# Kernel optimization log

Hardware: AMD Instinct MI355X
Metric: run time of the kernel (lower is better)

The kernel has to match this reference:

```python
import jax, jax.numpy as jnp
import numpy as np
from jax import lax

B, T, V, E, H, W = 4, 1024, 32000, 512, 1024, 8
EPS = 1e-5


def setup_inputs() -> dict:
    key = jax.random.key(0)
    ks = jax.random.split(key, 20)
    s = 0.05
    p = {
        'x': jax.random.randint(ks[0], (B, T), 0, V),
        'emb': jax.random.normal(ks[1], (V, E)) * s,
        # candidate_mlp: Linear(2H+E -> 2H), ReLU, Linear(2H -> H)
        'W1c': jax.random.normal(ks[2], (2 * H + E, 2 * H)) * s,
        'b1c': jnp.zeros((2 * H,)),
        'W2c': jax.random.normal(ks[3], (2 * H, H)) * s,
        'b2c': jnp.zeros((H,)),
        # gate_net: Linear(2H+E -> H), Tanh, Linear(H -> 1), Sigmoid
        'Wg1': jax.random.normal(ks[4], (2 * H + E, H)) * s,
        'bg1': jnp.zeros((H,)),
        'Wg2': jax.random.normal(ks[5], (H, 1)) * s,
        'bg2': jnp.zeros((1,)),
        # res_proj: Linear(E -> H)
        'Wr': jax.random.normal(ks[6], (E, H)) * s,
        'br': jnp.zeros((H,)),
        # attention projections (H -> H)
        'Wk': jax.random.normal(ks[7], (H, H)) * s,
        'bk': jnp.zeros((H,)),
        'Wq': jax.random.normal(ks[8], (H, H)) * s,
        'bq': jnp.zeros((H,)),
        'Wv': jax.random.normal(ks[9], (H, H)) * s,
        'bv': jnp.zeros((H,)),
        # output head (H -> V)
        'Wf': jax.random.normal(ks[10], (H, V)) * s,
        'bf': jnp.zeros((V,)),
    }
    return p


def _layer_norm(h):
    mu = h.mean(-1, keepdims=True)
    var = ((h - mu) ** 2).mean(-1, keepdims=True)
    return (h - mu) * lax.rsqrt(var + EPS)


def _forward(x, emb, W1c, b1c, W2c, b2c, Wg1, bg1, Wg2, bg2, Wr, br,
             Wk, bk, Wq, bq, Wv, bv, Wf, bf):
    e = emb[x]  # [B, T, E]
    h0 = jnp.zeros((B, H), dtype=e.dtype)

    def step(carry, et):
        h2, h1 = carry
        ctx = jnp.concatenate([h1, h2, et], axis=-1)  # [B, 2H+E]
        cand = jnp.maximum(ctx @ W1c + b1c, 0.0) @ W2c + b2c  # [B, H]
        gate = jax.nn.sigmoid(jnp.tanh(ctx @ Wg1 + bg1) @ Wg2 + bg2)  # [B, 1]
        h = h1 + gate * cand + 0.1 * (et @ Wr + br)
        hn = _layer_norm(h)
        return (h1, hn), hn

    _, states = lax.scan(step, (h0, h0), jnp.swapaxes(e, 0, 1))  # [T, B, H]
    states = jnp.swapaxes(states, 0, 1)  # [B, T, H]

    # windowed causal attention: each t attends to [max(0, t-W), t]
    q = states @ Wq + bq  # [B, T, H]
    k = states @ Wk + bk
    v = states @ Wv + bv
    t_idx = jnp.arange(T)[:, None]
    j = jnp.arange(W + 1)[None, :]
    idx = t_idx - W + j            # [T, W+1]
    valid = idx >= 0
    idxc = jnp.clip(idx, 0, T - 1)
    kw = k[:, idxc, :]             # [B, T, W+1, H]
    vw = v[:, idxc, :]
    scores = jnp.einsum('bth,btwh->btw', q, kw) / jnp.sqrt(jnp.asarray(H, q.dtype))
    scores = jnp.where(valid[None], scores, -jnp.inf)
    w = jax.nn.softmax(scores, axis=-1)
    attn = jnp.einsum('btw,btwh->bth', w, vw)  # [B, T, H]
    return attn @ Wf + bf  # [B, T, V]


def reference(x, emb, W1c, b1c, W2c, b2c, Wg1, bg1, Wg2, bg2, Wr, br,
              Wk, bk, Wq, bq, Wv, bv, Wf, bf):
    return _forward(x, emb, W1c, b1c, W2c, b2c, Wg1, bg1, Wg2, bg2, Wr, br,
                    Wk, bk, Wq, bq, Wv, bv, Wf, bf)
```

## Files before the change

kernel.cpp:

```cpp
#include <hip/hip_runtime.h>

typedef unsigned short ushort_t;

constexpr int TT = 1024;

__device__ __forceinline__ float blo(unsigned u) { return __uint_as_float(u << 16); }
__device__ __forceinline__ float bhi(unsigned u) { return __uint_as_float(u & 0xffff0000u); }
__device__ __forceinline__ ushort_t f2bf(float f) {
  unsigned u = __float_as_uint(f);
  unsigned r = (u + 0x7fffu + ((u >> 16) & 1u)) >> 16;
  return (ushort_t)r;
}
__device__ __forceinline__ float tanh_fast(float x) {
  float ax = fabsf(x);
  float e = exp2f(ax * 2.885390081777927f);
  float r = 1.f - 2.f / (e + 1.f);
  return copysignf(r, x);
}

__device__ __forceinline__ void st_agent(float* p, float v) {
  __hip_atomic_store(p, v, __ATOMIC_RELAXED, __HIP_MEMORY_SCOPE_AGENT);
}

__device__ __forceinline__ void ldg_hb4(const float* p0, const float* p1,
                                        const float* p2, const float* p3,
                                        float4& r0, float4& r1, float4& r2, float4& r3)
{
  asm volatile(
    "global_load_dwordx4 %0, %4, off sc0 sc1\n\t"
    "global_load_dwordx4 %1, %5, off sc0 sc1\n\t"
    "global_load_dwordx4 %2, %6, off sc0 sc1\n\t"
    "global_load_dwordx4 %3, %7, off sc0 sc1\n\t"
    "s_waitcnt vmcnt(0)"
    : "=&v"(r0), "=&v"(r1), "=&v"(r2), "=&v"(r3)
    : "v"(p0), "v"(p1), "v"(p2), "v"(p3)
    : "memory");
}

__device__ __forceinline__ void ldg_phase2(
    const float* gbase, const float* cbase,
    float4& g0, float4& g1, float4& g2, float4& g3,
    float4& a0, float4& a1, float4& a2, float4& a3,
    float4& a4, float4& a5, float4& a6, float4& a7)
{
  const float* cbase2 = cbase + 1024;
  asm volatile(
    "global_load_dwordx4 %0, %12, off sc0 sc1\n\t"
    "global_load_dwordx4 %1, %12, off offset:1024 sc0 sc1\n\t"
    "global_load_dwordx4 %2, %12, off offset:2048 sc0 sc1\n\t"
    "global_load_dwordx4 %3, %12, off offset:3072 sc0 sc1\n\t"
    "global_load_dwordx4 %4, %13, off sc0 sc1\n\t"
    "global_load_dwordx4 %5, %13, off offset:1024 sc0 sc1\n\t"
    "global_load_dwordx4 %6, %13, off offset:2048 sc0 sc1\n\t"
    "global_load_dwordx4 %7, %13, off offset:3072 sc0 sc1\n\t"
    "global_load_dwordx4 %8, %14, off sc0 sc1\n\t"
    "global_load_dwordx4 %9, %14, off offset:1024 sc0 sc1\n\t"
    "global_load_dwordx4 %10, %14, off offset:2048 sc0 sc1\n\t"
    "global_load_dwordx4 %11, %14, off offset:3072 sc0 sc1\n\t"
    "s_waitcnt vmcnt(0)"
    : "=&v"(g0), "=&v"(g1), "=&v"(g2), "=&v"(g3),
      "=&v"(a0), "=&v"(a1), "=&v"(a2), "=&v"(a3),
      "=&v"(a4), "=&v"(a5), "=&v"(a6), "=&v"(a7)
    : "v"(gbase), "v"(cbase), "v"(cbase2)
    : "memory");
}

__device__ __forceinline__ void gbar(unsigned* flags, int idx) {
  unsigned tgt = (unsigned)(idx + 1);
  __syncthreads();
  if (threadIdx.x == 0) {
    asm volatile("" ::: "memory");
    __hip_atomic_store(flags + ((size_t)blockIdx.x << 4), tgt,
                       __ATOMIC_RELAXED, __HIP_MEMORY_SCOPE_AGENT);
  }
  const unsigned* myf = flags + ((size_t)threadIdx.x << 4);
  while (__hip_atomic_load(myf, __ATOMIC_RELAXED, __HIP_MEMORY_SCOPE_AGENT) < tgt)
    __builtin_amdgcn_s_sleep(1);
  __syncthreads();
}

__global__ __launch_bounds__(256) void gemm_kernel(
    const float* __restrict__ A, const float* __restrict__ gA, const int* __restrict__ gidx,
    const float* __restrict__ W, int ldw,
    const float* __restrict__ bias, float scale,
    float* __restrict__ C, int M, int N, int K)
{
  __shared__ float As[16][68];
  __shared__ float Ws[16][68];
  int tid = threadIdx.x;
  int m0 = blockIdx.y * 64, n0 = blockIdx.x * 64;
  int tx = tid & 15, ty = tid >> 4;

  int am = tid >> 2;
  int ak = (tid & 3) << 2;
  int wk = tid >> 4;
  int wn = (tid & 15) << 2;
  int arow = m0 + am;
  const float* arow_p = (gidx != nullptr) ? &gA[(size_t)gidx[arow] * K] : &A[(size_t)arow * K];

  float acc[4][4];
#pragma unroll
  for (int i = 0; i < 4; ++i)
#pragma unroll
    for (int j = 0; j < 4; ++j) acc[i][j] = 0.f;

  for (int k0 = 0; k0 < K; k0 += 16) {
    float4 av = *(const float4*)&arow_p[k0 + ak];
    As[ak + 0][am] = av.x; As[ak + 1][am] = av.y;
    As[ak + 2][am] = av.z; As[ak + 3][am] = av.w;

    float4 wv = *(const float4*)&W[(size_t)(k0 + wk) * ldw + n0 + wn];
    Ws[wk][wn + 0] = wv.x; Ws[wk][wn + 1] = wv.y;
    Ws[wk][wn + 2] = wv.z; Ws[wk][wn + 3] = wv.w;
    __syncthreads();

#pragma unroll
    for (int kk = 0; kk < 16; ++kk) {
      float4 a4 = *(const float4*)&As[kk][ty << 2];
      float4 w4 = *(const float4*)&Ws[kk][tx << 2];
      float a_[4] = {a4.x, a4.y, a4.z, a4.w};
      float w_[4] = {w4.x, w4.y, w4.z, w4.w};
#pragma unroll
      for (int i = 0; i < 4; ++i)
#pragma unroll
        for (int j = 0; j < 4; ++j) acc[i][j] = fmaf(a_[i], w_[j], acc[i][j]);
    }
    __syncthreads();
  }

  int mbase = m0 + (ty << 2), nbase = n0 + (tx << 2);
  float bv4[4];
#pragma unroll
  for (int j = 0; j < 4; ++j) bv4[j] = bias[nbase + j];
#pragma unroll
  for (int i = 0; i < 4; ++i) {
    size_t ro = (size_t)(mbase + i) * N + nbase;
    float4 o;
    o.x = scale * (acc[i][0] + bv4[0]);
    o.y = scale * (acc[i][1] + bv4[1]);
    o.z = scale * (acc[i][2] + bv4[2]);
    o.w = scale * (acc[i][3] + bv4[3]);
    *(float4*)&C[ro] = o;
  }
}


constexpr int LDS_W1  = 0;
constexpr int LDS_W2  = 49152;
constexpr int LDS_WG2 = 65536;
constexpr int LDS_HN  = 67584;
constexpr int LDS_RED = 100352;
constexpr int LDS_B2  = 100608;
constexpr int RC_LDS_BYTES = 100624;

__global__ __launch_bounds__(256) void recur_kernel(
    const float* __restrict__ W1c, const float* __restrict__ Wg1,
    const float* __restrict__ W2c, const float* __restrict__ b2c,
    const float* __restrict__ Wg2, const float* __restrict__ bg2,
    const float* __restrict__ preA, const float* __restrict__ preG,
    const float* __restrict__ preR,
    float* __restrict__ states, float* __restrict__ ag,
    float* __restrict__ hbuf, unsigned* __restrict__ barcnt)
{
  extern __shared__ char lds[];
  ushort_t* w1   = (ushort_t*)(lds + LDS_W1);
  ushort_t* w2   = (ushort_t*)(lds + LDS_W2);
  ushort_t* wg2l = (ushort_t*)(lds + LDS_WG2);
  float*    hnf  = (float*)(lds + LDS_HN);
  float*    red  = (float*)(lds + LDS_RED);
  float*    b2l  = (float*)(lds + LDS_B2);

  int tid = threadIdx.x, bid = blockIdx.x;
  int ln = tid & 63, wv = tid >> 6;
  int j0 = bid * 12, j2 = bid << 2;

  for (int i = tid; i < 8192; i += 256) hnf[i] = 0.f;
  for (int i = tid; i < 12 * 2048; i += 256) {
    int c = i % 12, k = i / 12, j = j0 + c;
    float v = (j < 2048) ? W1c[(size_t)k * 2048 + j]
                         : Wg1[(size_t)k * 1024 + (j - 2048)];
    w1[c * 2048 + k] = f2bf(v);
  }
  for (int i = tid; i < 4 * 2048; i += 256) {
    int c = i & 3, k = i >> 2;
    w2[c * 2048 + k] = f2bf(W2c[(size_t)k * 1024 + j2 + c]);
  }
  for (int i = tid; i < 1024; i += 256) wg2l[i] = f2bf(Wg2[i]);
  if (tid < 4) b2l[tid] = b2c[j2 + tid];
  float bg2v = bg2[0];
  __syncthreads();

  int p = 0;

  for (int t = 0; t <= TT; ++t) {
    if (t > 0) {
      float4 xv[4]; float mu_[4], rs_[4];
      ldg_hb4(&hbuf[(0 << 10) + (tid << 2)], &hbuf[(1 << 10) + (tid << 2)],
              &hbuf[(2 << 10) + (tid << 2)], &hbuf[(3 << 10) + (tid << 2)],
              xv[0], xv[1], xv[2], xv[3]);
#pragma unroll
      for (int b = 0; b < 4; ++b) {
        float s  = xv[b].x + xv[b].y + xv[b].z + xv[b].w;
        float s2 = xv[b].x * xv[b].x + xv[b].y * xv[b].y + xv[b].z * xv[b].z + xv[b].w * xv[b].w;
#pragma unroll
        for (int off = 32; off; off >>= 1) { s += __shfl_xor(s, off); s2 += __shfl_xor(s2, off); }
        if (ln == 0) { red[(wv << 3) + (b << 1)] = s; red[(wv << 3) + (b << 1) + 1] = s2; }
      }
      __syncthreads();
#pragma unroll
      for (int b = 0; b < 4; ++b) {
        float s  = red[(b << 1)] + red[8 + (b << 1)] + red[16 + (b << 1)] + red[24 + (b << 1)];
        float s2 = red[(b << 1) + 1] + red[8 + (b << 1) + 1] + red[16 + (b << 1) + 1] + red[24 + (b << 1) + 1];
        float mu = s * (1.f / 1024.f);
        float var = s2 * (1.f / 1024.f) - mu * mu;
        mu_[b] = mu; rs_[b] = rsqrtf(var + 1e-5f);
      }
      int np = p ^ 1;
#pragma unroll
      for (int b = 0; b < 4; ++b) {
        float4 xn;
        xn.x = (xv[b].x - mu_[b]) * rs_[b];
        xn.y = (xv[b].y - mu_[b]) * rs_[b];
        xn.z = (xv[b].z - mu_[b]) * rs_[b];
        xn.w = (xv[b].w - mu_[b]) * rs_[b];
        *(float4*)&hnf[np * 4096 + (b << 10) + (tid << 2)] = xn;
        if (tid == bid)
          *(float4*)&states[((size_t)((b << 10) + (t - 1)) << 10) + (bid << 2)] = xn;
      }
      p = np;
      __syncthreads();
    }
    if (t == TT) break;

    {
      int b = wv;
      const float* pA = preA + ((size_t)((b << 10) + t) << 11);
      const float* pG = preG + ((size_t)((b << 10) + t) << 10);
      float pre = 0.f;
      if (ln < 12) {
        int j = j0 + ln;
        pre = (j < 2048) ? pA[j] : pG[j - 2048];
      }
      float acc[12];
#pragma unroll
      for (int c = 0; c < 12; ++c) acc[c] = 0.f;
      for (int k0 = 0; k0 < 2048; k0 += 256) {
        int kk = k0 + (ln << 2);
        int sel = (k0 < 1024) ? p : (p ^ 1);
        float4 hv = *(const float4*)&hnf[sel * 4096 + (b << 10) + (kk & 1023)];
#pragma unroll
        for (int c = 0; c < 12; ++c) {
          uint2 wq = *(const uint2*)&w1[c * 2048 + kk];
          float a = acc[c];
          a = fmaf(blo(wq.x), hv.x, a); a = fmaf(bhi(wq.x), hv.y, a);
          a = fmaf(blo(wq.y), hv.z, a); a = fmaf(bhi(wq.y), hv.w, a);
          acc[c] = a;
        }
      }
#pragma unroll
      for (int c = 0; c < 12; ++c) {
        float v = acc[c];
#pragma unroll
        for (int off = 32; off; off >>= 1) v += __shfl_xor(v, off);
        acc[c] = v;
      }
      if (ln < 12) {
        float v = acc[0];
#pragma unroll
        for (int c = 1; c < 12; ++c) if (ln == c) v = acc[c];
        st_agent(&ag[b * 3072 + j0 + ln], v + pre);
      }
    }
    gbar(barcnt, 2 * t);

    {
      int b = wv;
      const float* agv = ag + b * 3072;
      float pr = 0.f;
      if (ln < 4) pr = preR[((size_t)((b << 10) + t) << 10) + j2 + ln];

      float4 g0, g1, g2, g3, a0, a1, a2, a3, a4, a5, a6, a7;
      ldg_phase2(agv + 2048 + (ln << 2), agv + (ln << 2),
                 g0, g1, g2, g3, a0, a1, a2, a3, a4, a5, a6, a7);
      float4 gv_[4] = {g0, g1, g2, g3};
      float4 av_[8] = {a0, a1, a2, a3, a4, a5, a6, a7};

      float gs = 0.f;
#pragma unroll
      for (int i = 0; i < 4; ++i) {
        int gi = ((i << 6) + ln) << 2;
        uint2 wq = *(const uint2*)&wg2l[gi];
        gs = fmaf(tanh_fast(gv_[i].x), blo(wq.x), gs);
        gs = fmaf(tanh_fast(gv_[i].y), bhi(wq.x), gs);
        gs = fmaf(tanh_fast(gv_[i].z), blo(wq.y), gs);
        gs = fmaf(tanh_fast(gv_[i].w), bhi(wq.y), gs);
      }
#pragma unroll
      for (int off = 32; off; off >>= 1) gs += __shfl_xor(gs, off);
      float gate = 1.f / (1.f + exp2f(-1.4426950408889634f * (gs + bg2v)));

      float acc2[4] = {0.f, 0.f, 0.f, 0.f};
#pragma unroll
      for (int i = 0; i < 8; ++i) {
        int kk = (i << 8) + (ln << 2);
        float ax = fmaxf(av_[i].x, 0.f), ay = fmaxf(av_[i].y, 0.f);
        float az = fmaxf(av_[i].z, 0.f), aw = fmaxf(av_[i].w, 0.f);
#pragma unroll
        for (int c = 0; c < 4; ++c) {
          uint2 wq = *(const uint2*)&w2[c * 2048 + kk];
          float a = acc2[c];
          a = fmaf(blo(wq.x), ax, a); a = fmaf(bhi(wq.x), ay, a);
          a = fmaf(blo(wq.y), az, a); a = fmaf(bhi(wq.y), aw, a);
          acc2[c] = a;
        }
      }
#pragma unroll
      for (int c = 0; c < 4; ++c) {
        float v = acc2[c];
#pragma unroll
        for (int off = 32; off; off >>= 1) v += __shfl_xor(v, off);
        acc2[c] = v;
      }
      if (ln < 4) {
        float cand = acc2[0];
#pragma unroll
        for (int c = 1; c < 4; ++c) if (ln == c) cand = acc2[c];
        cand += b2l[ln];
        float h1v = hnf[p * 4096 + (b << 10) + j2 + ln];
        st_agent(&hbuf[(b << 10) + j2 + ln], h1v + gate * cand + pr);
      }
    }
    gbar(barcnt, 2 * t + 1);
  }
}

__global__ __launch_bounds__(256) void attn_kernel(
    const float* __restrict__ q, const float* __restrict__ kk,
    const float* __restrict__ vv, float* __restrict__ o)
{
  int m = blockIdx.x;
  int t = m & 1023;
  int tid = threadIdx.x;
  int ln = tid & 63, wvv = tid >> 6;
  int c0 = tid << 2;
  __shared__ float sred[36];

  float4 qv = *(const float4*)&q[((size_t)m << 10) + c0];
#pragma unroll
  for (int w = 0; w < 9; ++w) {
    int src = t + w - 8;
    float s = 0.f;
    if (src >= 0) {
      float4 kv = *(const float4*)&kk[((size_t)(m + w - 8) << 10) + c0];
      s = qv.x * kv.x + qv.y * kv.y + qv.z * kv.z + qv.w * kv.w;
    }
#pragma unroll
    for (int off = 32; off; off >>= 1) s += __shfl_xor(s, off);
    if (ln == 0) sred[w * 4 + wvv] = s;
  }
  __syncthreads();

  float p[9], mx = -3.4e38f;
#pragma unroll
  for (int w = 0; w < 9; ++w) {
    if (t + w - 8 >= 0) {
      float sc = (sred[w * 4] + sred[w * 4 + 1] + sred[w * 4 + 2] + sred[w * 4 + 3]) * 0.03125f;
      p[w] = sc; mx = fmaxf(mx, sc);
    } else p[w] = -3.4e38f;
  }
  float den = 0.f;
#pragma unroll
  for (int w = 0; w < 9; ++w) {
    float e = (t + w - 8 >= 0) ? exp2f(1.4426950408889634f * (p[w] - mx)) : 0.f;
    p[w] = e; den += e;
  }
  float inv = 1.f / den;
  float4 acc = {0.f, 0.f, 0.f, 0.f};
#pragma unroll
  for (int w = 0; w < 9; ++w) {
    if (t + w - 8 >= 0) {
      float4 vr = *(const float4*)&vv[((size_t)(m + w - 8) << 10) + c0];
      float pw = p[w] * inv;
      acc.x = fmaf(pw, vr.x, acc.x); acc.y = fmaf(pw, vr.y, acc.y);
      acc.z = fmaf(pw, vr.z, acc.z); acc.w = fmaf(pw, vr.w, acc.w);
    }
  }
  *(float4*)&o[((size_t)m << 10) + c0] = acc;
}

constexpr size_t OFF_STATES = 0;
constexpr size_t OFF_PREA   = 16777216;
constexpr size_t OFF_PREG   = 50331648;
constexpr size_t OFF_PRER   = 67108864;
constexpr size_t OFF_AG     = 83886080;
constexpr size_t OFF_HB     = 83935232;
constexpr size_t OFF_CNT    = 83951616;
constexpr size_t CNT_BYTES  = 16384;
constexpr size_t NEED_WS    = 83968000;

extern "C" void kernel_launch(void* const* d_in, const int* in_sizes, int n_in,
                              void* d_out, int out_size, void* d_ws, size_t ws_size,
                              hipStream_t stream) {
  const int*   x   = (const int*)d_in[0];
  const float* emb = (const float*)d_in[1];
  const float* W1c = (const float*)d_in[2];
  const float* b1c = (const float*)d_in[3];
  const float* W2c = (const float*)d_in[4];
  const float* b2c = (const float*)d_in[5];
  const float* Wg1 = (const float*)d_in[6];
  const float* bg1 = (const float*)d_in[7];
  const float* Wg2 = (const float*)d_in[8];
  const float* bg2 = (const float*)d_in[9];
  const float* Wr  = (const float*)d_in[10];
  const float* br  = (const float*)d_in[11];
  const float* Wk  = (const float*)d_in[12];
  const float* bk  = (const float*)d_in[13];
  const float* Wq  = (const float*)d_in[14];
  const float* bq  = (const float*)d_in[15];
  const float* Wv  = (const float*)d_in[16];
  const float* bv  = (const float*)d_in[17];
  const float* Wf  = (const float*)d_in[18];
  const float* bfv = (const float*)d_in[19];

  if (ws_size < NEED_WS) return;
  char* ws = (char*)d_ws;
  float* states = (float*)(ws + OFF_STATES);
  float* preA = (float*)(ws + OFF_PREA);
  float* preG = (float*)(ws + OFF_PREG);
  float* preR = (float*)(ws + OFF_PRER);
  float* agb  = (float*)(ws + OFF_AG);
  float* hbuf = (float*)(ws + OFF_HB);
  unsigned* barcnt = (unsigned*)(ws + OFF_CNT);

  dim3 blk(256);
  hipMemsetAsync(barcnt, 0, CNT_BYTES, stream);

  gemm_kernel<<<dim3(32, 64), blk, 0, stream>>>(nullptr, emb, x, W1c + (size_t)2048 * 2048, 2048,
                                                b1c, 1.f, preA, 4096, 2048, 512);
  gemm_kernel<<<dim3(16, 64), blk, 0, stream>>>(nullptr, emb, x, Wg1 + (size_t)2048 * 1024, 1024,
                                                bg1, 1.f, preG, 4096, 1024, 512);
  gemm_kernel<<<dim3(16, 64), blk, 0, stream>>>(nullptr, emb, x, Wr, 1024,
                                                br, 0.1f, preR, 4096, 1024, 512);

  hipFuncSetAttribute((const void*)recur_kernel,
                      hipFuncAttributeMaxDynamicSharedMemorySize, RC_LDS_BYTES);
  void* args[] = {(void*)&W1c, (void*)&Wg1, (void*)&W2c, (void*)&b2c, (void*)&Wg2, (void*)&bg2,
                  (void*)&preA, (void*)&preG, (void*)&preR,
                  (void*)&states, (void*)&agb, (void*)&hbuf, (void*)&barcnt};
  hipLaunchCooperativeKernel((const void*)recur_kernel, dim3(256), dim3(256),
                             args, RC_LDS_BYTES, stream);

  float* qb = preA;
  float* kb = preA + 4194304;
  float* vb = preG;
  float* ab = preR;
  gemm_kernel<<<dim3(16, 64), blk, 0, stream>>>(states, nullptr, nullptr, Wq, 1024,
                                                bq, 1.f, qb, 4096, 1024, 1024);
  gemm_kernel<<<dim3(16, 64), blk, 0, stream>>>(states, nullptr, nullptr, Wk, 1024,
                                                bk, 1.f, kb, 4096, 1024, 1024);
  gemm_kernel<<<dim3(16, 64), blk, 0, stream>>>(states, nullptr, nullptr, Wv, 1024,
                                                bv, 1.f, vb, 4096, 1024, 1024);
  attn_kernel<<<dim3(4096), blk, 0, stream>>>(qb, kb, vb, ab);
  gemm_kernel<<<dim3(500, 64), blk, 0, stream>>>(ab, nullptr, nullptr, Wf, 32000,
                                                 bfv, 1.f, (float*)d_out, 4096, 32000, 1024);
}
```

Baseline: 15.50 ms.

## Use split-bf16 MFMA GEMM for the vocabulary output projection

Replaces the FP32 SIMT GEMM for the final 4096x32000x1024 output head with a new kernel on bf16 matrix-core instructions. Each fp32 operand is split into high and low bf16 parts, and three MFMA products approximate fp32 accuracy. This targets the largest GEMM, which is likely a big share of total time. In exchange the per-tile fp32-to-bf16 split conversion in the load path, strided transposed LDS stores for B, and a small accuracy loss versus true fp32 add cost and risk.

```diff
diff --git a/kernel.cpp b/kernel.cpp
--- a/kernel.cpp
+++ b/kernel.cpp
@@ -1,6 +1,8 @@
 #include <hip/hip_runtime.h>
 
 typedef unsigned short ushort_t;
+typedef __attribute__((ext_vector_type(8))) short bf16x8;
+typedef __attribute__((ext_vector_type(4))) float f32x4;
 
 constexpr int TT = 1024;
 
@@ -144,6 +146,94 @@
   }
 }
 
+__global__ __launch_bounds__(256, 2) void mfma_gemm(
+    const float* __restrict__ A, const float* __restrict__ W,
+    const float* __restrict__ bias, float* __restrict__ C)
+{
+  __shared__ ushort_t Ah[128][40], Al[128][40], Bh[128][40], Bl[128][40];
+  int tid = threadIdx.x;
+  int bid = blockIdx.x;
+  int mb = bid & 31, nb = bid >> 5;
+  int m0 = mb << 7, n0 = nb << 7;
+  int l = tid & 63;
+  int wv = tid >> 6;
+  int wr = wv >> 1, wc = wv & 1;
+  int lr = l & 15, lg = l >> 4;
+
+  f32x4 acc[4][4];
+#pragma unroll
+  for (int i = 0; i < 4; ++i)
+#pragma unroll
+    for (int j = 0; j < 4; ++j) acc[i][j] = (f32x4){0.f, 0.f, 0.f, 0.f};
+
+  for (int k0 = 0; k0 < 1024; k0 += 32) {
+    __syncthreads();
+#pragma unroll
+    for (int r = 0; r < 4; ++r) {
+      int q = (r << 8) + tid;
+      int row = q >> 3, kq = q & 7;
+      float4 v = *(const float4*)&A[(size_t)(m0 + row) * 1024 + k0 + (kq << 2)];
+      float vv[4] = {v.x, v.y, v.z, v.w};
+      unsigned hw0, hw1, lw0, lw1;
+      {
+        ushort_t h0 = f2bf(vv[0]), h1 = f2bf(vv[1]), h2 = f2bf(vv[2]), h3 = f2bf(vv[3]);
+        ushort_t l0 = f2bf(vv[0] - blo(h0)), l1 = f2bf(vv[1] - blo(h1));
+        ushort_t l2 = f2bf(vv[2] - blo(h2)), l3 = f2bf(vv[3] - blo(h3));
+        hw0 = (unsigned)h0 | ((unsigned)h1 << 16); hw1 = (unsigned)h2 | ((unsigned)h3 << 16);
+        lw0 = (unsigned)l0 | ((unsigned)l1 << 16); lw1 = (unsigned)l2 | ((unsigned)l3 << 16);
+      }
+      *(uint2*)&Ah[row][kq << 2] = make_uint2(hw0, hw1);
+      *(uint2*)&Al[row][kq << 2] = make_uint2(lw0, lw1);
+    }
+#pragma unroll
+    for (int r = 0; r < 4; ++r) {
+      int q = (r << 8) + tid;
+      int wrow = q >> 5, nq = q & 31;
+      float4 v = *(const float4*)&W[(size_t)(k0 + wrow) * 32000 + n0 + (nq << 2)];
+      float vv[4] = {v.x, v.y, v.z, v.w};
+#pragma unroll
+      for (int e = 0; e < 4; ++e) {
+        ushort_t h = f2bf(vv[e]);
+        Bh[(nq << 2) + e][wrow] = h;
+        Bl[(nq << 2) + e][wrow] = f2bf(vv[e] - blo(h));
+      }
+    }
+    __syncthreads();
+
+    bf16x8 bh[4], bl[4];
+#pragma unroll
+    for (int j = 0; j < 4; ++j) {
+      int nrow = (wc << 6) + (j << 4) + lr;
+      bh[j] = *(const bf16x8*)&Bh[nrow][lg << 3];
+      bl[j] = *(const bf16x8*)&Bl[nrow][lg << 3];
+    }
+#pragma unroll
+    for (int i = 0; i < 4; ++i) {
+      int arow = (wr << 6) + (i << 4) + lr;
+      bf16x8 ah = *(const bf16x8*)&Ah[arow][lg << 3];
+      bf16x8 al = *(const bf16x8*)&Al[arow][lg << 3];
+#pragma unroll
+      for (int j = 0; j < 4; ++j) {
+        acc[i][j] = __builtin_amdgcn_mfma_f32_16x16x32_bf16(ah, bh[j], acc[i][j], 0, 0, 0);
+        acc[i][j] = __builtin_amdgcn_mfma_f32_16x16x32_bf16(ah, bl[j], acc[i][j], 0, 0, 0);
+        acc[i][j] = __builtin_amdgcn_mfma_f32_16x16x32_bf16(al, bh[j], acc[i][j], 0, 0, 0);
+      }
+    }
+  }
+
+#pragma unroll
+  for (int j = 0; j < 4; ++j) {
+    int n = n0 + (wc << 6) + (j << 4) + lr;
+    float bv = bias[n];
+#pragma unroll
+    for (int i = 0; i < 4; ++i) {
+      int mbase = m0 + (wr << 6) + (i << 4) + (lg << 2);
+#pragma unroll
+      for (int r = 0; r < 4; ++r)
+        C[(size_t)(mbase + r) * 32000 + n] = acc[i][j][r] + bv;
+    }
+  }
+}
 
 constexpr int LDS_W1  = 0;
 constexpr int LDS_W2  = 49152;
@@ -461,6 +551,5 @@
   gemm_kernel<<<dim3(16, 64), blk, 0, stream>>>(states, nullptr, nullptr, Wv, 1024,
                                                 bv, 1.f, vb, 4096, 1024, 1024);
   attn_kernel<<<dim3(4096), blk, 0, stream>>>(qb, kb, vb, ab);
-  gemm_kernel<<<dim3(500, 64), blk, 0, stream>>>(ab, nullptr, nullptr, Wf, 32000,
-                                                 bfv, 1.f, (float*)d_out, 4096, 32000, 1024);
-}
+  mfma_gemm<<<dim3(8000), blk, 0, stream>>>(ab, Wf, bfv, (float*)d_out);
+}
```

Measured after the change: 14.13 ms. 8.9% less time.
